# Kernel optimization log

Hardware: AMD Instinct MI355X
Metric: run time of the kernel (lower is better)

## Reference

```python
import jax, jax.numpy as jnp
import numpy as np

NUM_HEADS = 16
HEAD_DIM = 64
ROPE_BASE = 160000.0


def _rope_tables(seq_len, head_dim):
    inv_freq = 1.0 / (ROPE_BASE ** (jnp.arange(0, head_dim, 2, dtype=jnp.float32) / head_dim))
    freqs = jnp.arange(seq_len, dtype=jnp.float32)[:, None] * inv_freq[None, :]  # [S, hd/2]
    return jnp.cos(freqs)[None, None], jnp.sin(freqs)[None, None]  # [1,1,S,hd/2]


def _apply_rope(x, cos, sin):
    # x: [B, nh, S, hd]; split-half rotation as in the torch module
    x1, x2 = jnp.split(x, 2, axis=-1)
    return jnp.concatenate([x1 * cos - x2 * sin, x2 * cos + x1 * sin], axis=-1)


def setup_inputs() -> dict:
    key = jax.random.key(0)
    k1, k2, k3 = jax.random.split(key, 3)
    B, S, H = 2, 2048, 1024
    hidden_states = jax.random.normal(k1, (B, S, H), dtype=jnp.float32)
    # additive causal mask: 0 for allowed, -1e9 for future positions
    causal = jnp.tril(jnp.ones((S, S), dtype=bool))
    attention_mask = jnp.where(causal, 0.0, -1e9).astype(jnp.float32)[None, None]
    Wqkv = jax.random.normal(k2, (H, 3 * H), dtype=jnp.float32) * (H ** -0.5)
    Wo = jax.random.normal(k3, (H, H), dtype=jnp.float32) * (H ** -0.5)
    return {"hidden_states": hidden_states, "attention_mask": attention_mask, "Wqkv": Wqkv, "Wo": Wo}


def reference(hidden_states, attention_mask, Wqkv, Wo):
    B, S, H = hidden_states.shape
    nh, hd = NUM_HEADS, HEAD_DIM
    scale = hd ** -0.5

    qkv = hidden_states @ Wqkv                                   # [B,S,3H]
    qkv = qkv.reshape(B, S, 3, nh, hd).transpose(2, 0, 3, 1, 4)  # [3,B,nh,S,hd]
    q, k, v = qkv[0], qkv[1], qkv[2]

    cos, sin = _rope_tables(S, hd)
    q = _apply_rope(q, cos, sin)
    k = _apply_rope(k, cos, sin)

    scores = jnp.einsum('bhqd,bhkd->bhqk', q, k) * scale + attention_mask
    attn = jax.nn.softmax(scores, axis=-1)
    out = jnp.einsum('bhqk,bhkd->bhqd', attn, v)                 # [B,nh,S,hd]
    out = out.transpose(0, 2, 1, 3).reshape(B, S, H)
    return out @ Wo
```

## Files before the change

kernel.cpp:

```cpp
#include <hip/hip_runtime.h>
#include <hip/hip_bf16.h>

typedef __bf16 bf16x8 __attribute__((ext_vector_type(8)));
typedef float f32x4 __attribute__((ext_vector_type(4)));
typedef unsigned short u16;

__device__ __forceinline__ u16 f2bf(float f) {
    union { float f; unsigned u; } x{f};
    unsigned r = x.u + 0x7fffu + ((x.u >> 16) & 1u);
    return (u16)(r >> 16);
}
__device__ __forceinline__ unsigned pk2(float a, float b) {
    union { float f; unsigned u; } x{a}, y{b};
    return ((x.u + 0x8000u) >> 16) | ((y.u + 0x8000u) & 0xffff0000u);
}
__device__ __forceinline__ float ex2(float x) { return __builtin_amdgcn_exp2f(x); }
__device__ __forceinline__ f32x4 zero4() { f32x4 z = {0.f, 0.f, 0.f, 0.f}; return z; }

typedef const __attribute__((address_space(1))) unsigned int* gp1_t;
typedef __attribute__((address_space(3))) unsigned int* lp3_t;
__device__ __forceinline__ void async16(const u16* g, u16* l) {
    __builtin_amdgcn_global_load_lds((gp1_t)g, (lp3_t)l, 16, 0, 0);
}

__global__ void __launch_bounds__(256) prep(const float* __restrict__ hs,
                                            u16* __restrict__ Xb,
                                            const float* __restrict__ Wqkv,
                                            u16* __restrict__ Wqkvt,
                                            const float* __restrict__ Wo,
                                            u16* __restrict__ Wot,
                                            float* __restrict__ cosT,
                                            float* __restrict__ sinT) {
    __shared__ float tile[32][33];
    const int blk = blockIdx.x, t = threadIdx.x;
    if (blk < 4096) {
        int i = (blk * 256 + t) * 4;
        float4 v = *(const float4*)(hs + i);
        ushort4 o;
        o.x = f2bf(v.x); o.y = f2bf(v.y); o.z = f2bf(v.z); o.w = f2bf(v.w);
        *(ushort4*)(Xb + i) = o;
    } else if (blk < 8192) {
        const float* W; u16* Wt; int N, bx, by;
        if (blk < 7168) { int bid = blk - 4096; W = Wqkv; Wt = Wqkvt; N = 3072; bx = bid % 96; by = bid / 96; }
        else            { int bid = blk - 7168; W = Wo;   Wt = Wot;   N = 1024; bx = bid % 32; by = bid / 32; }
        const int K = 1024;
        int tx = t & 31, ty = t >> 5;
        int n0 = bx * 32, k0 = by * 32;
#pragma unroll
        for (int i = 0; i < 32; i += 8)
            tile[ty + i][tx] = W[(size_t)(k0 + ty + i) * N + n0 + tx];
        __syncthreads();
#pragma unroll
        for (int i = 0; i < 32; i += 8)
            Wt[(size_t)(n0 + ty + i) * K + k0 + tx] = f2bf(tile[tx][ty + i]);
    } else {
        int idx = (blk - 8192) * 256 + t;
        int d = idx & 31, s = idx >> 5;
        float inv = expf(-(float)d * 0.374466538f);
        float th = (float)s * inv;
        cosT[idx] = cosf(th);
        sinT[idx] = sinf(th);
    }
}

struct GemmCtx {
    f32x4 acc[4][4];
    int m16, q4, wm, wn;
};
template <int KDIM>
__device__ __forceinline__ void gemm_loop(const u16* __restrict__ A,
                                          const u16* __restrict__ Bt,
                                          int bm, int bn, GemmCtx& cx,
                                          u16* As, u16* Bs) {
    const int t = threadIdx.x;
    const int lane = t & 63, w = t >> 6;
    cx.wm = w >> 1; cx.wn = w & 1;
    cx.m16 = lane & 15; cx.q4 = lane >> 4;

    const int lrow = lane >> 2;
    const int kchunk = (lane & 3) ^ ((lane >> 3) & 3);
    const u16* Ag = A + (size_t)(bm * 128 + w * 32 + lrow) * KDIM + kchunk * 8;
    const u16* Bg = Bt + (size_t)(bn * 128 + w * 32 + lrow) * KDIM + kchunk * 8;
    const int l0 = (w * 32) * 32;
    const int l1 = (w * 32 + 16) * 32;
    const int kswz = (cx.q4 ^ ((cx.m16 >> 1) & 3)) * 8;

#pragma unroll
    for (int i = 0; i < 4; i++)
#pragma unroll
        for (int j = 0; j < 4; j++) cx.acc[i][j] = zero4();

    constexpr int NT = KDIM / 32;
    async16(Ag, As + l0);
    async16(Ag + 16 * KDIM, As + l1);
    async16(Bg, Bs + l0);
    async16(Bg + 16 * KDIM, Bs + l1);
    async16(Ag + 32, As + 4096 + l0);
    async16(Ag + 16 * KDIM + 32, As + 4096 + l1);
    async16(Bg + 32, Bs + 4096 + l0);
    async16(Bg + 16 * KDIM + 32, Bs + 4096 + l1);

    int co = 0, po = 2 * 4096;
#pragma unroll 1
    for (int tt = 0; tt < NT; ++tt) {
        if (tt + 1 < NT) {
            asm volatile("s_waitcnt vmcnt(4)" ::: "memory");
        } else {
            asm volatile("s_waitcnt vmcnt(0)" ::: "memory");
        }
        __builtin_amdgcn_s_barrier();
        __builtin_amdgcn_sched_barrier(0);
        if (tt + 2 < NT) {
            const int k0 = (tt + 2) * 32;
            async16(Ag + k0, As + po + l0);
            async16(Ag + 16 * KDIM + k0, As + po + l1);
            async16(Bg + k0, Bs + po + l0);
            async16(Bg + 16 * KDIM + k0, Bs + po + l1);
        }
        __builtin_amdgcn_sched_barrier(0);

        bf16x8 af[4], bf[4];
#pragma unroll
        for (int i = 0; i < 4; i++)
            af[i] = *(const bf16x8*)&As[co + (cx.wm * 64 + i * 16 + cx.m16) * 32 + kswz];
#pragma unroll
        for (int j = 0; j < 4; j++)
            bf[j] = *(const bf16x8*)&Bs[co + (cx.wn * 64 + j * 16 + cx.m16) * 32 + kswz];
#pragma unroll
        for (int i = 0; i < 4; i++)
#pragma unroll
            for (int j = 0; j < 4; j++)
                cx.acc[i][j] = __builtin_amdgcn_mfma_f32_16x16x32_bf16(af[i], bf[j], cx.acc[i][j], 0, 0, 0);

        asm volatile("" ::: "memory");
        __builtin_amdgcn_sched_barrier(0);
        co += 4096; if (co == 12288) co = 0;
        po += 4096; if (po == 12288) po = 0;
    }
}

struct GemmCtx3 {
    f32x4 acc[8][4];
    int m16, q4, wm, wn;
};
template <int KDIM>
__device__ __forceinline__ void gemm_loop3(const u16* __restrict__ A,
                                           const u16* __restrict__ Bt,
                                           int bm, int bn, GemmCtx3& cx,
                                           u16* As, u16* Bs) {
    const int t = threadIdx.x;
    const int lane = t & 63, w = t >> 6;
    cx.wm = w >> 2; cx.wn = w & 3;
    cx.m16 = lane & 15; cx.q4 = lane >> 4;

    const int srow = lane >> 3;
    const int schunk = (lane & 7) ^ (srow & 7);
    const u16* Ag = A + (size_t)(bm * 256 + w * 32 + srow) * KDIM + schunk * 8;
    const u16* Bg = Bt + (size_t)(bn * 256 + w * 32 + srow) * KDIM + schunk * 8;
    const int lb = (w * 32) * 64;

#pragma unroll
    for (int i = 0; i < 8; i++)
#pragma unroll
        for (int j = 0; j < 4; j++) cx.acc[i][j] = zero4();

    constexpr int NT = KDIM / 64;
    constexpr int HB = 256 * 64;

#pragma unroll
    for (int c = 0; c < 4; c++) {
        async16(Ag + c * 8 * KDIM, As + lb + c * 8 * 64);
        async16(Bg + c * 8 * KDIM, Bs + lb + c * 8 * 64);
    }

#pragma unroll 1
    for (int tt = 0; tt < NT; ++tt) {
        const int co = (tt & 1) * HB;
        if (tt + 1 < NT) {
            const int no = HB - co;
            const int k0 = (tt + 1) * 64;
#pragma unroll
            for (int c = 0; c < 4; c++) {
                async16(Ag + k0 + c * 8 * KDIM, As + no + lb + c * 8 * 64);
                async16(Bg + k0 + c * 8 * KDIM, Bs + no + lb + c * 8 * 64);
            }
            asm volatile("s_waitcnt vmcnt(8)" ::: "memory");
        } else {
            asm volatile("s_waitcnt vmcnt(0)" ::: "memory");
        }
        __builtin_amdgcn_s_barrier();
        asm volatile("" ::: "memory");
        __builtin_amdgcn_sched_barrier(0);

        const int m7 = cx.m16 & 7;
#pragma unroll
        for (int ks = 0; ks < 2; ks++) {
            const int slot = ((ks * 4 + cx.q4) ^ m7) * 8;
            bf16x8 af[8], bf[4];
#pragma unroll
            for (int i = 0; i < 8; i++)
                af[i] = *(const bf16x8*)&As[co + (cx.wm * 128 + i * 16 + cx.m16) * 64 + slot];
#pragma unroll
            for (int j = 0; j < 4; j++)
                bf[j] = *(const bf16x8*)&Bs[co + (cx.wn * 64 + j * 16 + cx.m16) * 64 + slot];
#pragma unroll
            for (int i = 0; i < 8; i++)
#pragma unroll
                for (int j = 0; j < 4; j++)
                    cx.acc[i][j] = __builtin_amdgcn_mfma_f32_16x16x32_bf16(af[i], bf[j], cx.acc[i][j], 0, 0, 0);
        }

        asm volatile("" ::: "memory");
        __builtin_amdgcn_sched_barrier(0);
        __builtin_amdgcn_s_barrier();
    }
}

__global__ void __launch_bounds__(512, 2) gemm_qkv(const u16* __restrict__ A,
                                                   const u16* __restrict__ Bt,
                                                   const float* __restrict__ cosT,
                                                   const float* __restrict__ sinT,
                                                   u16* __restrict__ Q,
                                                   u16* __restrict__ Kd,
                                                   u16* __restrict__ Vt) {
    __shared__ __align__(16) u16 As[2 * 256 * 64];
    __shared__ __align__(16) u16 Bs[2 * 256 * 64];
    GemmCtx3 cx;
    const int hw = blockIdx.x;
    const int orig = (hw & 7) * 24 + (hw >> 3);
    const int bm = orig / 12, bn = orig % 12;
    gemm_loop3<1024>(A, Bt, bm, bn, cx, As, Bs);
    const int m16 = cx.m16, q4 = cx.q4;

    const int colbase = bn * 256 + cx.wn * 64;
    const int type = colbase >> 10;
    const int h = (colbase & 1023) >> 6;
    const int rbase = bm * 256 + cx.wm * 128;

    if (type == 2) {
#pragma unroll
        for (int i = 0; i < 8; i++) {
            int s0 = rbase + i * 16 + q4 * 4;
            int b = s0 >> 11, sl = s0 & 2047;
            size_t ob = (size_t)(b * 16 + h) * 64 * 2048;
#pragma unroll
            for (int j = 0; j < 4; j++) {
                int d = j * 16 + m16;
                ushort4 o;
                o.x = f2bf(cx.acc[i][j][0]);
                o.y = f2bf(cx.acc[i][j][1]);
                o.z = f2bf(cx.acc[i][j][2]);
                o.w = f2bf(cx.acc[i][j][3]);
                *(ushort4*)&Vt[ob + (size_t)d * 2048 + sl] = o;
            }
        }
    } else {
        u16* dst = (type == 0) ? Q : Kd;
        const float qs = (type == 0) ? 0.1803368801f  : 1.0f;
#pragma unroll
        for (int i = 0; i < 8; i++)
#pragma unroll
            for (int rr = 0; rr < 4; rr++) {
                int r = rbase + i * 16 + q4 * 4 + rr;
                int b = r >> 11, s = r & 2047;
                size_t ob = ((size_t)((b * 16 + h) * 2048 + s)) * 64;
#pragma unroll
                for (int j2 = 0; j2 < 2; j2++) {
                    int d = j2 * 16 + m16;
                    float cs = cosT[s * 32 + d];
                    float sn = sinT[s * 32 + d];
                    float x1 = cx.acc[i][j2][rr];
                    float x2 = cx.acc[i][j2 + 2][rr];
                    dst[ob + d]      = f2bf((x1 * cs - x2 * sn) * qs);
                    dst[ob + d + 32] = f2bf((x2 * cs + x1 * sn) * qs);
                }
            }
    }
}

__global__ void __launch_bounds__(256) gemm_out(const u16* __restrict__ A,
                                                const u16* __restrict__ Bt,
                                                float* __restrict__ C) {
    __shared__ __align__(16) u16 As[3 * 128 * 32];
    __shared__ __align__(16) u16 Bs[3 * 128 * 32];
    GemmCtx cx;
    const int bm = blockIdx.y, bn = blockIdx.x;
    gemm_loop<1024>(A, Bt, bm, bn, cx, As, Bs);
    const int N = 1024;
#pragma unroll
    for (int i = 0; i < 4; i++)
#pragma unroll
        for (int j = 0; j < 4; j++)
#pragma unroll
            for (int rr = 0; rr < 4; rr++) {
                int row = bm * 128 + cx.wm * 64 + i * 16 + cx.q4 * 4 + rr;
                int col = bn * 128 + cx.wn * 64 + j * 16 + cx.m16;
                C[(size_t)row * N + col] = cx.acc[i][j][rr];
            }
}

__global__ void __launch_bounds__(512) attn_kernel(const u16* __restrict__ Q,
                                                   const u16* __restrict__ Kg_,
                                                   const u16* __restrict__ Vtg_,
                                                   u16* __restrict__ O) {
    __shared__ __align__(16) u16 Ks[2][64][72];
    __shared__ __align__(16) u16 Vs[2][64][72];
    __shared__ __align__(16) u16 Pt[8][16][72];
    const int t = threadIdx.x, w = t >> 6;
    const int m16 = t & 15, q4 = (t & 63) >> 4;
    const int bx = blockIdx.x, bh = blockIdx.y;
    const size_t base = (size_t)bh * 2048 * 64;
    const int b = bh >> 4, h = bh & 15;
    const int skey = t >> 3, sc = (t & 7) * 8;

#pragma unroll 1
    for (int ph = 0; ph < 2; ph++) {
        const int st = ph ? (15 - bx) : bx;
        const int qrow = st * 128 + w * 16 + m16;
        const u16* Qg = Q + base + (size_t)qrow * 64;
        bf16x8 qf0 = *(const bf16x8*)(Qg + q4 * 8);
        bf16x8 qf1 = *(const bf16x8*)(Qg + 32 + q4 * 8);

        f32x4 occ[4];
#pragma unroll
        for (int dc = 0; dc < 4; dc++) occ[dc] = zero4();
        float li = 0.f;

        const int jtmax = 2 * st + 1;
        const int jd = 2 * st + (w >> 2);

        const u16* Kb0 = Kg_ + base + skey * 64 + sc;
        const u16* Vt0 = Vtg_ + base + (size_t)skey * 2048 + sc;
        uint4 ka = *(const uint4*)(Kb0);
        uint4 va = *(const uint4*)(Vt0);

#pragma unroll 1
        for (int jt = 0; jt <= jtmax; jt++) {
            const int bi = jt & 1;
            *(uint4*)&Ks[bi][skey][sc] = ka;
            *(uint4*)&Vs[bi][skey][sc] = va;
            if (jt < jtmax) {
                ka = *(const uint4*)(Kb0 + (size_t)(jt + 1) * 4096);
                va = *(const uint4*)(Vt0 + (size_t)(jt + 1) * 64);
            }
            __syncthreads();

            if (jt <= jd) {
                f32x4 stv[4];
#pragma unroll
                for (int c = 0; c < 4; c++) stv[c] = zero4();
#pragma unroll
                for (int c = 0; c < 4; c++) {
                    bf16x8 kf0 = *(const bf16x8*)&Ks[bi][c * 16 + m16][q4 * 8];
                    bf16x8 kf1 = *(const bf16x8*)&Ks[bi][c * 16 + m16][32 + q4 * 8];
                    stv[c] = __builtin_amdgcn_mfma_f32_16x16x32_bf16(kf0, qf0, stv[c], 0, 0, 0);
                    stv[c] = __builtin_amdgcn_mfma_f32_16x16x32_bf16(kf1, qf1, stv[c], 0, 0, 0);
                }

                float pv[4][4];
#pragma unroll
                for (int c = 0; c < 4; c++)
#pragma unroll
                    for (int rr = 0; rr < 4; rr++) pv[c][rr] = stv[c][rr];
                if (jt == jd) {
                    const int ql = qrow - 64 * jt;
#pragma unroll
                    for (int c = 0; c < 4; c++)
#pragma unroll
                        for (int rr = 0; rr < 4; rr++)
                            if (c * 16 + q4 * 4 + rr > ql) pv[c][rr] = -1e30f;
                }

#pragma unroll
                for (int c = 0; c < 4; c++) {
                    float p0 = ex2(pv[c][0] - 24.f);
                    float p1 = ex2(pv[c][1] - 24.f);
                    float p2 = ex2(pv[c][2] - 24.f);
                    float p3 = ex2(pv[c][3] - 24.f);
                    li += (p0 + p1) + (p2 + p3);
                    *(uint2*)&Pt[w][m16][c * 16 + q4 * 4] = make_uint2(pk2(p0, p1), pk2(p2, p3));
                }

#pragma unroll
                for (int ks = 0; ks < 2; ks++) {
                    bf16x8 pf = *(const bf16x8*)&Pt[w][m16][ks * 32 + q4 * 8];
#pragma unroll
                    for (int dc = 0; dc < 4; dc++) {
                        bf16x8 vf = *(const bf16x8*)&Vs[bi][dc * 16 + m16][ks * 32 + q4 * 8];
                        occ[dc] = __builtin_amdgcn_mfma_f32_16x16x32_bf16(vf, pf, occ[dc], 0, 0, 0);
                    }
                }
            }
        }

        li += __shfl_xor(li, 16);
        li += __shfl_xor(li, 32);
        float rli = 1.0f / li;
        u16* Op = O + ((size_t)(b * 2048 + qrow)) * 1024 + h * 64 + q4 * 4;
#pragma unroll
        for (int dc = 0; dc < 4; dc++) {
            ushort4 o;
            o.x = f2bf(occ[dc][0] * rli);
            o.y = f2bf(occ[dc][1] * rli);
            o.z = f2bf(occ[dc][2] * rli);
            o.w = f2bf(occ[dc][3] * rli);
            *(ushort4*)(Op + dc * 16) = o;
        }
        __syncthreads();
    }
}

extern "C" void kernel_launch(void* const* d_in, const int* in_sizes, int n_in,
                              void* d_out, int out_size, void* d_ws, size_t ws_size,
                              hipStream_t stream) {
    const float* hs   = (const float*)d_in[0];
    const float* Wqkv = (const float*)d_in[2];
    const float* Wo   = (const float*)d_in[3];
    float* out = (float*)d_out;

    const int BS = 4096;
    const int H = 1024, N3 = 3072;
    const int SH = 32 * 2048 * 64;

    u16* Xb    = (u16*)d_ws;
    u16* Wqkvt = Xb + (size_t)BS * H;
    u16* Wot   = Wqkvt + (size_t)N3 * H;
    u16* Qb    = Wot + (size_t)H * H;
    u16* Kb    = Qb + SH;
    u16* Vtb   = Kb + SH;
    u16* AOb   = Vtb + SH;
    float* cosT = (float*)(AOb + (size_t)BS * H);
    float* sinT = cosT + 2048 * 32;

    prep<<<8448, 256, 0, stream>>>(hs, Xb, Wqkv, Wqkvt, Wo, Wot, cosT, sinT);

    gemm_qkv<<<192, 512, 0, stream>>>(Xb, Wqkvt, cosT, sinT, Qb, Kb, Vtb);

    attn_kernel<<<dim3(8, 32), 512, 0, stream>>>(Qb, Kb, Vtb, AOb);

    gemm_out<<<dim3(H / 128, BS / 128), 256, 0, stream>>>(AOb, Wot, out);
}
```

Before: 191.8 us.

## Restructure QKV GEMM main loop into four-phase ping-pong with split staging

Replaces the QKV GEMM mainloop with a four-phase schedule. Each phase loads one half of the A or B operand fragments, issues the async global-to-LDS copy for the next tile's half, then runs eight MFMAs between barriers with raised wave priority. Each wave now owns 64-row quadrants, split into low and high halves, instead of 128 contiguous rows. The prep kernel permutes Wqkv columns so each wave's accumulator columns still line up with the per-head RoPE pairing. The aim is finer interleaving of memory traffic and MFMA work to hide load latency, at the cost of more barriers and a more fragile staging and waitcnt schedule.

```diff
diff --git a/kernel.cpp b/kernel.cpp
--- a/kernel.cpp
+++ b/kernel.cpp
@@ -41,8 +41,9 @@
         *(ushort4*)(Xb + i) = o;
     } else if (blk < 8192) {
         const float* W; u16* Wt; int N, bx, by;
-        if (blk < 7168) { int bid = blk - 4096; W = Wqkv; Wt = Wqkvt; N = 3072; bx = bid % 96; by = bid / 96; }
-        else            { int bid = blk - 7168; W = Wo;   Wt = Wot;   N = 1024; bx = bid % 32; by = bid / 32; }
+        bool qkv = (blk < 7168);
+        if (qkv) { int bid = blk - 4096; W = Wqkv; Wt = Wqkvt; N = 3072; bx = bid % 96; by = bid / 96; }
+        else     { int bid = blk - 7168; W = Wo;   Wt = Wot;   N = 1024; bx = bid % 32; by = bid / 32; }
         const int K = 1024;
         int tx = t & 31, ty = t >> 5;
         int n0 = bx * 32, k0 = by * 32;
@@ -51,8 +52,15 @@
             tile[ty + i][tx] = W[(size_t)(k0 + ty + i) * N + n0 + tx];
         __syncthreads();
 #pragma unroll
-        for (int i = 0; i < 32; i += 8)
-            Wt[(size_t)(n0 + ty + i) * K + k0 + tx] = f2bf(tile[tx][ty + i]);
+        for (int i = 0; i < 32; i += 8) {
+            int n = n0 + ty + i;
+            int np = n;
+            if (qkv) {
+                int hh = (n >> 6) & 3, f = (n >> 4) & 3;
+                np = (n & ~255) | (((f >> 1) * 8 + hh * 2 + (f & 1)) << 4) | (n & 15);
+            }
+            Wt[(size_t)np * K + k0 + tx] = f2bf(tile[tx][ty + i]);
+        }
     } else {
         int idx = (blk - 8192) * 256 + t;
         int d = idx & 31, s = idx >> 5;
@@ -139,83 +147,6 @@
     }
 }
 
-struct GemmCtx3 {
-    f32x4 acc[8][4];
-    int m16, q4, wm, wn;
-};
-template <int KDIM>
-__device__ __forceinline__ void gemm_loop3(const u16* __restrict__ A,
-                                           const u16* __restrict__ Bt,
-                                           int bm, int bn, GemmCtx3& cx,
-                                           u16* As, u16* Bs) {
-    const int t = threadIdx.x;
-    const int lane = t & 63, w = t >> 6;
-    cx.wm = w >> 2; cx.wn = w & 3;
-    cx.m16 = lane & 15; cx.q4 = lane >> 4;
-
-    const int srow = lane >> 3;
-    const int schunk = (lane & 7) ^ (srow & 7);
-    const u16* Ag = A + (size_t)(bm * 256 + w * 32 + srow) * KDIM + schunk * 8;
-    const u16* Bg = Bt + (size_t)(bn * 256 + w * 32 + srow) * KDIM + schunk * 8;
-    const int lb = (w * 32) * 64;
-
-#pragma unroll
-    for (int i = 0; i < 8; i++)
-#pragma unroll
-        for (int j = 0; j < 4; j++) cx.acc[i][j] = zero4();
-
-    constexpr int NT = KDIM / 64;
-    constexpr int HB = 256 * 64;
-
-#pragma unroll
-    for (int c = 0; c < 4; c++) {
-        async16(Ag + c * 8 * KDIM, As + lb + c * 8 * 64);
-        async16(Bg + c * 8 * KDIM, Bs + lb + c * 8 * 64);
-    }
-
-#pragma unroll 1
-    for (int tt = 0; tt < NT; ++tt) {
-        const int co = (tt & 1) * HB;
-        if (tt + 1 < NT) {
-            const int no = HB - co;
-            const int k0 = (tt + 1) * 64;
-#pragma unroll
-            for (int c = 0; c < 4; c++) {
-                async16(Ag + k0 + c * 8 * KDIM, As + no + lb + c * 8 * 64);
-                async16(Bg + k0 + c * 8 * KDIM, Bs + no + lb + c * 8 * 64);
-            }
-            asm volatile("s_waitcnt vmcnt(8)" ::: "memory");
-        } else {
-            asm volatile("s_waitcnt vmcnt(0)" ::: "memory");
-        }
-        __builtin_amdgcn_s_barrier();
-        asm volatile("" ::: "memory");
-        __builtin_amdgcn_sched_barrier(0);
-
-        const int m7 = cx.m16 & 7;
-#pragma unroll
-        for (int ks = 0; ks < 2; ks++) {
-            const int slot = ((ks * 4 + cx.q4) ^ m7) * 8;
-            bf16x8 af[8], bf[4];
-#pragma unroll
-            for (int i = 0; i < 8; i++)
-                af[i] = *(const bf16x8*)&As[co + (cx.wm * 128 + i * 16 + cx.m16) * 64 + slot];
-#pragma unroll
-            for (int j = 0; j < 4; j++)
-                bf[j] = *(const bf16x8*)&Bs[co + (cx.wn * 64 + j * 16 + cx.m16) * 64 + slot];
-#pragma unroll
-            for (int i = 0; i < 8; i++)
-#pragma unroll
-                for (int j = 0; j < 4; j++)
-                    cx.acc[i][j] = __builtin_amdgcn_mfma_f32_16x16x32_bf16(af[i], bf[j], cx.acc[i][j], 0, 0, 0);
-        }
-
-        asm volatile("" ::: "memory");
-        __builtin_amdgcn_sched_barrier(0);
-        __builtin_amdgcn_s_barrier();
-    }
-}
-
 __global__ void __launch_bounds__(512, 2) gemm_qkv(const u16* __restrict__ A,
                                                    const u16* __restrict__ Bt,
                                                    const float* __restrict__ cosT,
@@ -225,32 +156,134 @@
                                                    u16* __restrict__ Vt) {
     __shared__ __align__(16) u16 As[2 * 256 * 64];
     __shared__ __align__(16) u16 Bs[2 * 256 * 64];
-    GemmCtx3 cx;
+    constexpr int HB = 256 * 64;
+    const int t = threadIdx.x, lane = t & 63, w = t >> 6;
+    const int wm = w >> 2, wn = w & 3;
+    const int m16 = lane & 15, q4 = lane >> 4, m7 = m16 & 7;
     const int hw = blockIdx.x;
     const int orig = (hw & 7) * 24 + (hw >> 3);
     const int bm = orig / 12, bn = orig % 12;
-    gemm_loop3<1024>(A, Bt, bm, bn, cx, As, Bs);
-    const int m16 = cx.m16, q4 = cx.q4;
-
-    const int colbase = bn * 256 + cx.wn * 64;
+
+    const int srow = lane >> 3;
+    const int schunk = (lane & 7) ^ srow;
+    const u16* Ag = A + (size_t)(bm * 256 + w * 8 + srow) * 1024 + schunk * 8;
+    const u16* Bg = Bt + (size_t)(bn * 256 + w * 8 + srow) * 1024 + schunk * 8;
+    u16* AsW = As + w * 512;
+    u16* BsW = Bs + w * 512;
+
+    f32x4 acc[8][4];
+#pragma unroll
+    for (int i = 0; i < 8; i++)
+#pragma unroll
+        for (int j = 0; j < 4; j++) acc[i][j] = zero4();
+
+    const int slt0 = (q4 ^ m7) * 8;
+    const int slt1 = ((4 + q4) ^ m7) * 8;
+
+#define STGA(S, H) do { const u16* g_ = Ag + (size_t)(H) * 131072 + (S) * 64; \
+    u16* l_ = AsW + ((S) & 1) * HB + (H) * 8192; \
+    async16(g_, l_); async16(g_ + 65536, l_ + 4096); } while (0)
+#define STGB(S, H) do { const u16* g_ = Bg + (size_t)(H) * 131072 + (S) * 64; \
+    u16* l_ = BsW + ((S) & 1) * HB + (H) * 8192; \
+    async16(g_, l_); async16(g_ + 65536, l_ + 4096); } while (0)
+
+    STGA(0, 0); STGB(0, 0); STGA(0, 1); STGB(0, 1); STGA(1, 0); STGB(1, 0);
+    asm volatile("s_waitcnt vmcnt(4)" ::: "memory");
+    __builtin_amdgcn_sched_barrier(0);
+    __builtin_amdgcn_s_barrier();
+
+#define MFMA8(IB, B0, B1) do { \
+    _Pragma("unroll") for (int i4 = 0; i4 < 4; i4++) \
+    _Pragma("unroll") for (int j2 = 0; j2 < 2; j2++) \
+        acc[(IB) + i4][(JB) + j2] = __builtin_amdgcn_mfma_f32_16x16x32_bf16(a0[i4], B0[j2], acc[(IB) + i4][(JB) + j2], 0, 0, 0); \
+    _Pragma("unroll") for (int i4 = 0; i4 < 4; i4++) \
+    _Pragma("unroll") for (int j2 = 0; j2 < 2; j2++) \
+        acc[(IB) + i4][(JB) + j2] = __builtin_amdgcn_mfma_f32_16x16x32_bf16(a1[i4], B1[j2], acc[(IB) + i4][(JB) + j2], 0, 0, 0); \
+} while (0)
+
+#define BAR1() do { __builtin_amdgcn_sched_barrier(0); __builtin_amdgcn_s_barrier(); \
+                    __builtin_amdgcn_s_setprio(1); } while (0)
+#define BAR2() do { __builtin_amdgcn_s_setprio(0); asm volatile("" ::: "memory"); \
+                    __builtin_amdgcn_sched_barrier(0); __builtin_amdgcn_s_barrier(); } while (0)
+
+#pragma unroll 1
+    for (int T = 0; T < 16; ++T) {
+        const int co = (T & 1) * HB;
+        const int aL = co + (wm * 64 + m16) * 64;
+        const int aH = aL + 128 * 64;
+        const int bL = co + (wn * 32 + m16) * 64;
+        const int bH = bL + 128 * 64;
+        bf16x8 a0[4], a1[4], pl0[2], pl1[2], ph0[2], ph1[2];
+
+#pragma unroll
+        for (int i4 = 0; i4 < 4; i4++) {
+            a0[i4] = *(const bf16x8*)&As[aL + i4 * 1024 + slt0];
+            a1[i4] = *(const bf16x8*)&As[aL + i4 * 1024 + slt1];
+        }
+#pragma unroll
+        for (int j2 = 0; j2 < 2; j2++) {
+            pl0[j2] = *(const bf16x8*)&Bs[bL + j2 * 1024 + slt0];
+            pl1[j2] = *(const bf16x8*)&Bs[bL + j2 * 1024 + slt1];
+        }
+        if (T < 15) STGA(T + 1, 1);
+        BAR1();
+        { constexpr int JB = 0; MFMA8(0, pl0, pl1); }
+        BAR2();
+
+#pragma unroll
+        for (int j2 = 0; j2 < 2; j2++) {
+            ph0[j2] = *(const bf16x8*)&Bs[bH + j2 * 1024 + slt0];
+            ph1[j2] = *(const bf16x8*)&Bs[bH + j2 * 1024 + slt1];
+        }
+        if (T < 15) STGB(T + 1, 1);
+        BAR1();
+        { constexpr int JB = 2; MFMA8(0, ph0, ph1); }
+        BAR2();
+
+#pragma unroll
+        for (int i4 = 0; i4 < 4; i4++) {
+            a0[i4] = *(const bf16x8*)&As[aH + i4 * 1024 + slt0];
+            a1[i4] = *(const bf16x8*)&As[aH + i4 * 1024 + slt1];
+        }
+        if (T < 14) STGA(T + 2, 0);
+        BAR1();
+        { constexpr int JB = 0; MFMA8(4, pl0, pl1); }
+        BAR2();
+
+        if (T < 14) {
+            STGB(T + 2, 0);
+            asm volatile("s_waitcnt vmcnt(4)" ::: "memory");
+        } else {
+            asm volatile("s_waitcnt vmcnt(0)" ::: "memory");
+        }
+        BAR1();
+        { constexpr int JB = 2; MFMA8(4, ph0, ph1); }
+        BAR2();
+    }
+#undef STGA
+#undef STGB
+#undef MFMA8
+#undef BAR1
+#undef BAR2
+
+    const int colbase = bn * 256 + wn * 64;
     const int type = colbase >> 10;
     const int h = (colbase & 1023) >> 6;
-    const int rbase = bm * 256 + cx.wm * 128;
 
     if (type == 2) {
 #pragma unroll
         for (int i = 0; i < 8; i++) {
-            int s0 = rbase + i * 16 + q4 * 4;
-            int b = s0 >> 11, sl = s0 & 2047;
+            int sr = bm * 256 + (i >> 2) * 128 + wm * 64 + (i & 3) * 16 + q4 * 4;
+            int b = sr >> 11, sl = sr & 2047;
             size_t ob = (size_t)(b * 16 + h) * 64 * 2048;
 #pragma unroll
             for (int j = 0; j < 4; j++) {
                 int d = j * 16 + m16;
                 ushort4 o;
-                o.x = f2bf(cx.acc[i][j][0]);
-                o.y = f2bf(cx.acc[i][j][1]);
-                o.z = f2bf(cx.acc[i][j][2]);
-                o.w = f2bf(cx.acc[i][j][3]);
+                o.x = f2bf(acc[i][j][0]);
+                o.y = f2bf(acc[i][j][1]);
+                o.z = f2bf(acc[i][j][2]);
+                o.w = f2bf(acc[i][j][3]);
                 *(ushort4*)&Vt[ob + (size_t)d * 2048 + sl] = o;
             }
         }
@@ -261,7 +294,7 @@
         for (int i = 0; i < 8; i++)
 #pragma unroll
             for (int rr = 0; rr < 4; rr++) {
-                int r = rbase + i * 16 + q4 * 4 + rr;
+                int r = bm * 256 + (i >> 2) * 128 + wm * 64 + (i & 3) * 16 + q4 * 4 + rr;
                 int b = r >> 11, s = r & 2047;
                 size_t ob = ((size_t)((b * 16 + h) * 2048 + s)) * 64;
 #pragma unroll
@@ -269,8 +302,8 @@
                     int d = j2 * 16 + m16;
                     float cs = cosT[s * 32 + d];
                     float sn = sinT[s * 32 + d];
-                    float x1 = cx.acc[i][j2][rr];
-                    float x2 = cx.acc[i][j2 + 2][rr];
+                    float x1 = acc[i][j2][rr];
+                    float x2 = acc[i][j2 + 2][rr];
                     dst[ob + d]      = f2bf((x1 * cs - x2 * sn) * qs);
                     dst[ob + d + 32] = f2bf((x2 * cs + x1 * sn) * qs);
                 }
```

New measurement: 189.5 us. About the same (-1.2%).
